# Optimization experiments

Measured on AMD Instinct MI355X. Metric: run time of the kernel, lower is better.

## Reference

```python
import jax, jax.numpy as jnp
from jax import lax
import numpy as np

N_FEATURE = 128
EDGE = 12          # int(sqrt(128) + 1)
BATCH = 131072


def maxpool2(x):
    # 2x2 max pool, stride 2, NCHW
    return lax.reduce_window(x, -jnp.inf, lax.max,
                             (1, 1, 2, 2), (1, 1, 2, 2), 'VALID')


def conv3x3(x, w, b):
    # 3x3 conv, padding=1, NCHW / OIHW
    y = lax.conv_general_dilated(x, w, window_strides=(1, 1),
                                 padding=((1, 1), (1, 1)),
                                 dimension_numbers=('NCHW', 'OIHW', 'NCHW'))
    return y + b[None, :, None, None]


def setup_inputs() -> dict:
    key = jax.random.key(0)
    ks = jax.random.split(key, 9)
    x = jax.random.normal(ks[0], (BATCH, N_FEATURE), dtype=jnp.float32)
    conv1_w = jax.random.normal(ks[1], (3, 1, 3, 3), dtype=jnp.float32) * 0.1
    conv1_b = jnp.zeros((3,), dtype=jnp.float32)
    conv2_w = jax.random.normal(ks[2], (6, 3, 3, 3), dtype=jnp.float32) * 0.1
    conv2_b = jnp.zeros((6,), dtype=jnp.float32)
    fc1_w = jax.random.normal(ks[3], (128, 54), dtype=jnp.float32) * 0.1
    fc1_b = jnp.zeros((128,), dtype=jnp.float32)
    out_w = jax.random.normal(ks[4], (N_FEATURE, 128), dtype=jnp.float32) * 0.1
    out_b = jnp.zeros((N_FEATURE,), dtype=jnp.float32)
    return {"x": x, "conv1_w": conv1_w, "conv1_b": conv1_b,
            "conv2_w": conv2_w, "conv2_b": conv2_b,
            "fc1_w": fc1_w, "fc1_b": fc1_b,
            "out_w": out_w, "out_b": out_b}


def reference(x, conv1_w, conv1_b, conv2_w, conv2_b, fc1_w, fc1_b, out_w, out_b):
    num = x.shape[0]
    n = x.shape[1]                       # 128
    pad = EDGE * EDGE - n                # 16 trailing zeros
    # vectorized transto3D: row-major fill of edge x edge grid, zero-padded tail
    g = jnp.pad(x, ((0, 0), (0, pad))).reshape(num, 1, EDGE, EDGE)
    h = jax.nn.relu(maxpool2(conv3x3(g, conv1_w, conv1_b)))      # [num,3,6,6]
    h = jax.nn.relu(maxpool2(conv3x3(h, conv2_w, conv2_b)))      # [num,6,3,3]
    h = h.reshape(num, 54)
    h = jax.nn.relu(h @ fc1_w.T + fc1_b)                         # [num,128]
    return h @ out_w.T + out_b                                   # [num,128]
```

## Files before the change

### kernel.cpp

```cpp
#include <hip/hip_runtime.h>

typedef unsigned int uint;
typedef unsigned short ushort;

using bf16x8 = __attribute__((ext_vector_type(8))) short;
using f32x4  = __attribute__((ext_vector_type(4))) float;

__device__ __forceinline__ float b2f(ushort u) {
  union { uint i; float f; } v; v.i = ((uint)u) << 16; return v.f;
}
__device__ __forceinline__ ushort f2b(float f) {
  union { float f; uint i; } v; v.f = f;
  uint r = (v.i + 0x7fffu + ((v.i >> 16) & 1u)) >> 16;
  return (ushort)r;
}
__device__ __forceinline__ bf16x8 ldfrag(const ushort* p) {
  union { uint4 u; bf16x8 v; } x; x.u = *(const uint4*)p; return x.v;
}
__device__ __forceinline__ bf16x8 pack8(const float4 a, const float4 b) {
  union { uint4 u; bf16x8 v; } x;
  x.u.x = (uint)f2b(a.x) | ((uint)f2b(a.y) << 16);
  x.u.y = (uint)f2b(a.z) | ((uint)f2b(a.w) << 16);
  x.u.z = (uint)f2b(b.x) | ((uint)f2b(b.y) << 16);
  x.u.w = (uint)f2b(b.z) | ((uint)f2b(b.w) << 16);
  return x.v;
}

template <int Q>
__device__ __forceinline__ void conv_sample(
    const float* __restrict__ xs,
    const float* __restrict__ w1g, const float* __restrict__ b1g,
    const float* __restrict__ w2g, const float* __restrict__ b2g,
    ushort* __restrict__ strow) {
  constexpr int HRLO = (Q == 0) ? 0 : (Q == 1) ? 1 : 3;
  constexpr int HRHI = (Q == 0) ? 2 : (Q == 1) ? 4 : 5;
  constexpr int NR = HRHI - HRLO + 1;
  constexpr int F4LO = (Q == 0) ? 0 : (Q == 1) ? 3 : 15;
  constexpr int F4HI = (Q == 0) ? 20 : 31;

  float xv[128];
#pragma unroll
  for (int i = F4LO; i <= F4HI; ++i) {
    const float4 v = ((const float4*)xs)[i];
    xv[4 * i + 0] = v.x; xv[4 * i + 1] = v.y;
    xv[4 * i + 2] = v.z; xv[4 * i + 3] = v.w;
  }

  float w1[3][9], b1[3];
#pragma unroll
  for (int c = 0; c < 3; ++c) {
    b1[c] = b1g[c];
#pragma unroll
    for (int q = 0; q < 9; ++q) w1[c][q] = w1g[c * 9 + q];
  }

  float h1[3][NR][6];
#pragma unroll
  for (int ri = 0; ri < NR; ++ri) {
    const int hr = HRLO + ri;
#pragma unroll
    for (int pc = 0; pc < 6; ++pc)
#pragma unroll
      for (int ch = 0; ch < 3; ++ch) {
        float m = -3.0e38f;
#pragma unroll
        for (int dr = 0; dr < 2; ++dr)
#pragma unroll
          for (int dc = 0; dc < 2; ++dc) {
            float a = 0.f;
#pragma unroll
            for (int ky = 0; ky < 3; ++ky)
#pragma unroll
              for (int kx = 0; kx < 3; ++kx) {
                const int r = 2 * hr + dr + ky - 1;
                const int c = 2 * pc + dc + kx - 1;
                if (r >= 0 && r < 12 && c >= 0 && c < 12 && (12 * r + c) < 128)
                  a = fmaf(w1[ch][ky * 3 + kx], xv[12 * r + c], a);
              }
            m = fmaxf(m, a);
          }
        h1[ch][ri][pc] = fmaxf(m + b1[ch], 0.f);
      }
  }

#pragma unroll
  for (int o = 0; o < 6; ++o) {
    float w2[27];
#pragma unroll
    for (int q = 0; q < 27; ++q) w2[q] = w2g[o * 27 + q];
    const float bo = b2g[o];
#pragma unroll
    for (int qc = 0; qc < 3; ++qc) {
      float m = -3.0e38f;
#pragma unroll
      for (int dr = 0; dr < 2; ++dr)
#pragma unroll
        for (int dc = 0; dc < 2; ++dc) {
          float a = 0.f;
#pragma unroll
          for (int i = 0; i < 3; ++i)
#pragma unroll
            for (int ky = 0; ky < 3; ++ky)
#pragma unroll
              for (int kx = 0; kx < 3; ++kx) {
                const int yy = 2 * Q + dr + ky - 1;
                const int xx = 2 * qc + dc + kx - 1;
                if (yy >= HRLO && yy <= HRHI && xx >= 0 && xx < 6)
                  a = fmaf(w2[i * 9 + ky * 3 + kx], h1[i][yy - HRLO][xx], a);
              }
          m = fmaxf(m, a);
        }
      strow[o * 9 + Q * 3 + qc] = f2b(fmaxf(m + bo, 0.f));
    }
  }
  if (Q == 2) {
    uint* p = (uint*)(strow + 54);
#pragma unroll
    for (int q = 0; q < 5; ++q) p[q] = 0u;
  }
}

__global__ __launch_bounds__(384, 4) void conv_kernel_r8(
    const float* __restrict__ x,
    const float* __restrict__ w1g, const float* __restrict__ b1g,
    const float* __restrict__ w2g, const float* __restrict__ b2g,
    ushort* __restrict__ h2ws) {
  __shared__ ushort h2st[128][66];

  const int t = threadIdx.x;
  const int s0 = blockIdx.x * 128;
  const int wv = t >> 6;
  const int q  = (wv < 3) ? wv : wv - 3;
  const int sg = (wv < 3) ? 0 : 1;
  const int si = sg * 64 + (t & 63);

  const float* xs = x + (size_t)(s0 + si) * 128;
  ushort* strow = &h2st[si][0];

  if (q == 0)      conv_sample<0>(xs, w1g, b1g, w2g, b2g, strow);
  else if (q == 1) conv_sample<1>(xs, w1g, b1g, w2g, b2g, strow);
  else             conv_sample<2>(xs, w1g, b1g, w2g, b2g, strow);

  __syncthreads();

#pragma unroll
  for (int i = 0; i < 11; ++i) {
    const int f = t + 384 * i;
    if (f < 4096) {
      const int sr = f >> 5, dw = f & 31;
      const uint v = *(const uint*)&h2st[sr][dw * 2];
      ((uint*)h2ws)[((size_t)(s0 + sr) << 5) + dw] = v;
    }
  }
}

__global__ __launch_bounds__(256, 3) void fc_kernel_r8(
    const ushort* __restrict__ h2ws,
    const float* __restrict__ fc1w, const float* __restrict__ fc1b,
    const float* __restrict__ outw, const float* __restrict__ outb,
    float* __restrict__ out) {
  __shared__ __align__(16) ushort w1s[128][72];
  __shared__ __align__(16) ushort tA[128][132];
  __shared__ __align__(16) float fb1[128];
  __shared__ __align__(16) float ob[128];

  const int t = threadIdx.x;
  const int s0 = blockIdx.x * 128;
  const int lane = t & 63, wv = t >> 6;
  const int quad = lane >> 4, lm = lane & 15;

  bf16x8 bh[2][8];
#pragma unroll
  for (int st = 0; st < 8; ++st) {
    const ushort* rp = h2ws + (size_t)(s0 + 16 * st + lm) * 64 + quad * 8;
    bh[0][st] = ldfrag(rp);
    bh[1][st] = ldfrag(rp + 32);
  }

  if (t < 128) { fb1[t] = fc1b[t]; ob[t] = outb[t]; }

#pragma unroll
  for (int i = 0; i < 27; ++i) {
    const int f = t + 256 * i;
    const int n = f / 54, k = f - 54 * n;
    w1s[n][k] = f2b(fc1w[f]);
  }
  if (t < 128) {
    uint* p = (uint*)&w1s[t][54];
#pragma unroll
    for (int q = 0; q < 5; ++q) p[q] = 0u;
  }
  __syncthreads();

  f32x4 acc[2][8];
#pragma unroll
  for (int mt = 0; mt < 2; ++mt)
#pragma unroll
    for (int st = 0; st < 8; ++st) acc[mt][st] = (f32x4){0.f, 0.f, 0.f, 0.f};

#pragma unroll
  for (int kk = 0; kk < 2; ++kk) {
    const int ko = kk * 32 + quad * 8;
    bf16x8 aw[2];
#pragma unroll
    for (int mt = 0; mt < 2; ++mt)
      aw[mt] = ldfrag(&w1s[32 * wv + 16 * mt + lm][ko]);
#pragma unroll
    for (int mt = 0; mt < 2; ++mt)
#pragma unroll
      for (int st = 0; st < 8; ++st)
        acc[mt][st] = __builtin_amdgcn_mfma_f32_16x16x32_bf16(
            aw[mt], bh[kk][st], acc[mt][st], 0, 0, 0);
  }

#pragma unroll
  for (int mt = 0; mt < 2; ++mt) {
    const int jb = 32 * wv + 16 * mt + quad * 4;
    const float4 bj = *(const float4*)&fb1[jb];
#pragma unroll
    for (int st = 0; st < 8; ++st) {
      const int sR = 16 * st + lm;
      const float v0 = fmaxf(acc[mt][st][0] + bj.x, 0.f);
      const float v1 = fmaxf(acc[mt][st][1] + bj.y, 0.f);
      const float v2 = fmaxf(acc[mt][st][2] + bj.z, 0.f);
      const float v3 = fmaxf(acc[mt][st][3] + bj.w, 0.f);
      uint2 pv;
      pv.x = (uint)f2b(v0) | ((uint)f2b(v1) << 16);
      pv.y = (uint)f2b(v2) | ((uint)f2b(v3) << 16);
      *(uint2*)&tA[sR][jb] = pv;
    }
  }
  __syncthreads();

  f32x4 acc2[2][8];
#pragma unroll
  for (int mt = 0; mt < 2; ++mt)
#pragma unroll
    for (int st = 0; st < 8; ++st) acc2[mt][st] = (f32x4){0.f, 0.f, 0.f, 0.f};

#pragma unroll
  for (int kk = 0; kk < 4; ++kk) {
    const int ko = kk * 32 + quad * 8;
    bf16x8 ao[2], bt[8];
#pragma unroll
    for (int mt = 0; mt < 2; ++mt) {
      const float* rp = outw + (size_t)(32 * wv + 16 * mt + lm) * 128 + ko;
      const float4 v0 = *(const float4*)rp;
      const float4 v1 = *(const float4*)(rp + 4);
      ao[mt] = pack8(v0, v1);
    }
#pragma unroll
    for (int st = 0; st < 8; ++st)
      bt[st] = ldfrag(&tA[16 * st + lm][ko]);
#pragma unroll
    for (int mt = 0; mt < 2; ++mt)
#pragma unroll
      for (int st = 0; st < 8; ++st)
        acc2[mt][st] = __builtin_amdgcn_mfma_f32_16x16x32_bf16(
            ao[mt], bt[st], acc2[mt][st], 0, 0, 0);
  }

#pragma unroll
  for (int mt = 0; mt < 2; ++mt) {
    const int obase = 32 * wv + 16 * mt + quad * 4;
    const float4 b4 = *(const float4*)&ob[obase];
#pragma unroll
    for (int st = 0; st < 8; ++st) {
      const int srow = s0 + 16 * st + lm;
      float4 o4;
      o4.x = acc2[mt][st][0] + b4.x;
      o4.y = acc2[mt][st][1] + b4.y;
      o4.z = acc2[mt][st][2] + b4.z;
      o4.w = acc2[mt][st][3] + b4.w;
      *(float4*)&out[(size_t)srow * 128 + obase] = o4;
    }
  }
}

extern "C" void kernel_launch(void* const* d_in, const int* in_sizes, int n_in,
                              void* d_out, int out_size, void* d_ws, size_t ws_size,
                              hipStream_t stream) {
  const float* x    = (const float*)d_in[0];
  const float* w1   = (const float*)d_in[1];
  const float* b1   = (const float*)d_in[2];
  const float* w2   = (const float*)d_in[3];
  const float* b2   = (const float*)d_in[4];
  const float* fc1w = (const float*)d_in[5];
  const float* fc1b = (const float*)d_in[6];
  const float* outw = (const float*)d_in[7];
  const float* outb = (const float*)d_in[8];
  float* outp = (float*)d_out;
  ushort* ws  = (ushort*)d_ws;

  const int N = in_sizes[0] / 128;

  conv_kernel_r8<<<N / 128, 384, 0, stream>>>(x, w1, b1, w2, b2, ws);
  fc_kernel_r8<<<N / 128, 256, 0, stream>>>(ws, fc1w, fc1b, outw, outb, outp);
}
```

Measured before the change: 205.6 us.

## Split conv work by channel across thread groups with LDS-staged conv1 output

Conv work is now split by output channel instead of by output row band. Each of three 128-thread groups computes one conv1 channel for all samples and streams input rows through a rolling 4-row register window. The results go to LDS, and after a barrier each group computes two conv2 output channels. This removes the redundant conv1 recomputation and the large per-thread 128-float input array of the old row-split scheme. In exchange it needs a large LDS buffer (about 56KB plus staging) and an extra barrier, and lowers the occupancy hint from 4 to 3 blocks.

```diff
diff --git a/kernel.cpp b/kernel.cpp
--- a/kernel.cpp
+++ b/kernel.cpp
@@ -26,121 +26,178 @@
   return x.v;
 }
 
-template <int Q>
-__device__ __forceinline__ void conv_sample(
-    const float* __restrict__ xs,
-    const float* __restrict__ w1g, const float* __restrict__ b1g,
-    const float* __restrict__ w2g, const float* __restrict__ b2g,
-    ushort* __restrict__ strow) {
-  constexpr int HRLO = (Q == 0) ? 0 : (Q == 1) ? 1 : 3;
-  constexpr int HRHI = (Q == 0) ? 2 : (Q == 1) ? 4 : 5;
-  constexpr int NR = HRHI - HRLO + 1;
-  constexpr int F4LO = (Q == 0) ? 0 : (Q == 1) ? 3 : 15;
-  constexpr int F4HI = (Q == 0) ? 20 : 31;
-
-  float xv[128];
-#pragma unroll
-  for (int i = F4LO; i <= F4HI; ++i) {
-    const float4 v = ((const float4*)xs)[i];
-    xv[4 * i + 0] = v.x; xv[4 * i + 1] = v.y;
-    xv[4 * i + 2] = v.z; xv[4 * i + 3] = v.w;
-  }
-
-  float w1[3][9], b1[3];
-#pragma unroll
-  for (int c = 0; c < 3; ++c) {
-    b1[c] = b1g[c];
-#pragma unroll
-    for (int q = 0; q < 9; ++q) w1[c][q] = w1g[c * 9 + q];
-  }
-
-  float h1[3][NR][6];
-#pragma unroll
-  for (int ri = 0; ri < NR; ++ri) {
-    const int hr = HRLO + ri;
-#pragma unroll
-    for (int pc = 0; pc < 6; ++pc)
-#pragma unroll
-      for (int ch = 0; ch < 3; ++ch) {
-        float m = -3.0e38f;
-#pragma unroll
-        for (int dr = 0; dr < 2; ++dr)
-#pragma unroll
-          for (int dc = 0; dc < 2; ++dc) {
-            float a = 0.f;
-#pragma unroll
-            for (int ky = 0; ky < 3; ++ky)
-#pragma unroll
-              for (int kx = 0; kx < 3; ++kx) {
-                const int r = 2 * hr + dr + ky - 1;
-                const int c = 2 * pc + dc + kx - 1;
-                if (r >= 0 && r < 12 && c >= 0 && c < 12 && (12 * r + c) < 128)
-                  a = fmaf(w1[ch][ky * 3 + kx], xv[12 * r + c], a);
-              }
-            m = fmaxf(m, a);
+template <int R>
+__device__ __forceinline__ void load_row(const float* __restrict__ xs,
+                                         float (&d)[12]) {
+  if constexpr (R >= 11) {
+#pragma unroll
+    for (int c = 0; c < 12; ++c) d[c] = 0.f;
+  } else if constexpr (R == 10) {
+    const float4 a = *(const float4*)(xs + 120);
+    const float4 b = *(const float4*)(xs + 124);
+    d[0] = a.x; d[1] = a.y; d[2] = a.z; d[3] = a.w;
+    d[4] = b.x; d[5] = b.y; d[6] = b.z; d[7] = b.w;
+    d[8] = 0.f; d[9] = 0.f; d[10] = 0.f; d[11] = 0.f;
+  } else {
+#pragma unroll
+    for (int q = 0; q < 3; ++q) {
+      const float4 v = *(const float4*)(xs + 12 * R + 4 * q);
+      d[4 * q + 0] = v.x; d[4 * q + 1] = v.y;
+      d[4 * q + 2] = v.z; d[4 * q + 3] = v.w;
+    }
+  }
+}
+
+template <int PR>
+__device__ __forceinline__ void conv1_band(const float* __restrict__ xs,
+                                           float (&xr)[4][12],
+                                           const float (&w1r)[9], float b1v,
+                                           float* __restrict__ hlrow) {
+  if constexpr (PR >= 1) {
+    load_row<2 * PR + 1>(xs, xr[(2 * PR + 1) & 3]);
+    if constexpr (2 * PR + 2 <= 11)
+      load_row<2 * PR + 2>(xs, xr[(2 * PR + 2) & 3]);
+  }
+  float out[6];
+#pragma unroll
+  for (int pc = 0; pc < 6; ++pc) {
+    float m = -3.0e38f;
+#pragma unroll
+    for (int dr = 0; dr < 2; ++dr)
+#pragma unroll
+      for (int dc = 0; dc < 2; ++dc) {
+        float a = 0.f;
+#pragma unroll
+        for (int ky = 0; ky < 3; ++ky)
+#pragma unroll
+          for (int kx = 0; kx < 3; ++kx) {
+            const int y = 2 * PR + dr + ky - 1;
+            const int cc = 2 * pc + dc + kx - 1;
+            if (y >= 0 && y < 12 && cc >= 0 && cc < 12 &&
+                (12 * y + cc) < 128)
+              a = fmaf(w1r[ky * 3 + kx], xr[y & 3][cc], a);
           }
-        h1[ch][ri][pc] = fmaxf(m + b1[ch], 0.f);
+        m = fmaxf(m, a);
       }
-  }
-
-#pragma unroll
-  for (int o = 0; o < 6; ++o) {
-    float w2[27];
-#pragma unroll
-    for (int q = 0; q < 27; ++q) w2[q] = w2g[o * 27 + q];
-    const float bo = b2g[o];
-#pragma unroll
-    for (int qc = 0; qc < 3; ++qc) {
-      float m = -3.0e38f;
-#pragma unroll
-      for (int dr = 0; dr < 2; ++dr)
-#pragma unroll
-        for (int dc = 0; dc < 2; ++dc) {
-          float a = 0.f;
-#pragma unroll
-          for (int i = 0; i < 3; ++i)
-#pragma unroll
-            for (int ky = 0; ky < 3; ++ky)
-#pragma unroll
-              for (int kx = 0; kx < 3; ++kx) {
-                const int yy = 2 * Q + dr + ky - 1;
-                const int xx = 2 * qc + dc + kx - 1;
-                if (yy >= HRLO && yy <= HRHI && xx >= 0 && xx < 6)
-                  a = fmaf(w2[i * 9 + ky * 3 + kx], h1[i][yy - HRLO][xx], a);
-              }
-          m = fmaxf(m, a);
-        }
-      strow[o * 9 + Q * 3 + qc] = f2b(fmaxf(m + bo, 0.f));
-    }
-  }
-  if (Q == 2) {
-    uint* p = (uint*)(strow + 54);
-#pragma unroll
-    for (int q = 0; q < 5; ++q) p[q] = 0u;
-  }
-}
-
-__global__ __launch_bounds__(384, 4) void conv_kernel_r8(
+    out[pc] = fmaxf(m + b1v, 0.f);
+  }
+#pragma unroll
+  for (int q = 0; q < 3; ++q)
+    *(float2*)&hlrow[PR * 6 + 2 * q] = make_float2(out[2 * q], out[2 * q + 1]);
+}
+
+__global__ __launch_bounds__(384, 3) void conv_kernel_r9(
     const float* __restrict__ x,
     const float* __restrict__ w1g, const float* __restrict__ b1g,
     const float* __restrict__ w2g, const float* __restrict__ b2g,
     ushort* __restrict__ h2ws) {
+  __shared__ float hl[128 * 110];
   __shared__ ushort h2st[128][66];
 
   const int t = threadIdx.x;
   const int s0 = blockIdx.x * 128;
-  const int wv = t >> 6;
-  const int q  = (wv < 3) ? wv : wv - 3;
-  const int sg = (wv < 3) ? 0 : 1;
-  const int si = sg * 64 + (t & 63);
+  const int si = t & 127;
+  const int grp = __builtin_amdgcn_readfirstlane(t >> 7);
 
   const float* xs = x + (size_t)(s0 + si) * 128;
-  ushort* strow = &h2st[si][0];
-
-  if (q == 0)      conv_sample<0>(xs, w1g, b1g, w2g, b2g, strow);
-  else if (q == 1) conv_sample<1>(xs, w1g, b1g, w2g, b2g, strow);
-  else             conv_sample<2>(xs, w1g, b1g, w2g, b2g, strow);
-
+
+  {
+    float w1r[9];
+#pragma unroll
+    for (int q = 0; q < 9; ++q) w1r[q] = w1g[grp * 9 + q];
+    const float b1v = b1g[grp];
+
+    float xr[4][12];
+    load_row<0>(xs, xr[0]);
+    load_row<1>(xs, xr[1]);
+    load_row<2>(xs, xr[2]);
+    float* hlrow = &hl[si * 110 + grp * 36];
+
+    conv1_band<0>(xs, xr, w1r, b1v, hlrow);
+    conv1_band<1>(xs, xr, w1r, b1v, hlrow);
+    conv1_band<2>(xs, xr, w1r, b1v, hlrow);
+    conv1_band<3>(xs, xr, w1r, b1v, hlrow);
+    conv1_band<4>(xs, xr, w1r, b1v, hlrow);
+    conv1_band<5>(xs, xr, w1r, b1v, hlrow);
+  }
+  __syncthreads();
+
+  {
+    const int o0 = 2 * grp;
+    float w2a[27], w2b[27];
+#pragma unroll
+    for (int q = 0; q < 27; ++q) {
+      w2a[q] = w2g[o0 * 27 + q];
+      w2b[q] = w2g[(o0 + 1) * 27 + q];
+    }
+    const float b2a = b2g[o0], b2b = b2g[o0 + 1];
+    const float* hbase = &hl[si * 110];
+
+#pragma unroll
+    for (int qr = 0; qr < 3; ++qr) {
+      const int lo = (qr == 0) ? 0 : 2 * qr - 1;
+      const int hi = (qr == 2) ? 5 : 2 * qr + 2;
+      float s[2][3][4];
+#pragma unroll
+      for (int oo = 0; oo < 2; ++oo)
+#pragma unroll
+        for (int qc = 0; qc < 3; ++qc)
+#pragma unroll
+          for (int p = 0; p < 4; ++p) s[oo][qc][p] = 0.f;
+
+#pragma unroll
+      for (int i = 0; i < 3; ++i) {
+        float hwv[4][6];
+#pragma unroll
+        for (int rr = 0; rr < 4; ++rr) {
+          if (lo + rr <= hi) {
+#pragma unroll
+            for (int q = 0; q < 3; ++q) {
+              const float2 p2 =
+                  *(const float2*)&hbase[i * 36 + (lo + rr) * 6 + 2 * q];
+              hwv[rr][2 * q] = p2.x; hwv[rr][2 * q + 1] = p2.y;
+            }
+          }
+        }
+#pragma unroll
+        for (int ky = 0; ky < 3; ++ky)
+#pragma unroll
+          for (int kx = 0; kx < 3; ++kx) {
+            const float wa = w2a[i * 9 + ky * 3 + kx];
+            const float wb = w2b[i * 9 + ky * 3 + kx];
+#pragma unroll
+            for (int dr = 0; dr < 2; ++dr) {
+              const int y = 2 * qr + dr + ky - 1;
+              if (y < lo || y > hi) continue;
+#pragma unroll
+              for (int qc = 0; qc < 3; ++qc)
+#pragma unroll
+                for (int dc = 0; dc < 2; ++dc) {
+                  const int xx = 2 * qc + dc + kx - 1;
+                  if (xx < 0 || xx > 5) continue;
+                  const float h = hwv[y - lo][xx];
+                  s[0][qc][dr * 2 + dc] = fmaf(wa, h, s[0][qc][dr * 2 + dc]);
+                  s[1][qc][dr * 2 + dc] = fmaf(wb, h, s[1][qc][dr * 2 + dc]);
+                }
+            }
+          }
+      }
+#pragma unroll
+      for (int oo = 0; oo < 2; ++oo)
+#pragma unroll
+        for (int qc = 0; qc < 3; ++qc) {
+          const float m = fmaxf(fmaxf(s[oo][qc][0], s[oo][qc][1]),
+                                fmaxf(s[oo][qc][2], s[oo][qc][3]));
+          const float bv = oo ? b2b : b2a;
+          h2st[si][(o0 + oo) * 9 + qr * 3 + qc] = f2b(fmaxf(m + bv, 0.f));
+        }
+    }
+    if (grp == 2) {
+      uint* p = (uint*)&h2st[si][54];
+#pragma unroll
+      for (int q = 0; q < 5; ++q) p[q] = 0u;
+    }
+  }
   __syncthreads();
 
 #pragma unroll
@@ -154,7 +211,7 @@
   }
 }
 
-__global__ __launch_bounds__(256, 3) void fc_kernel_r8(
+__global__ __launch_bounds__(256, 3) void fc_kernel_r9(
     const ushort* __restrict__ h2ws,
     const float* __restrict__ fc1w, const float* __restrict__ fc1b,
     const float* __restrict__ outw, const float* __restrict__ outb,
@@ -294,6 +351,6 @@
 
   const int N = in_sizes[0] / 128;
 
-  conv_kernel_r8<<<N / 128, 384, 0, stream>>>(x, w1, b1, w2, b2, ws);
-  fc_kernel_r8<<<N / 128, 256, 0, stream>>>(ws, fc1w, fc1b, outw, outb, outp);
-}
+  conv_kernel_r9<<<N / 128, 384, 0, stream>>>(x, w1, b1, w2, b2, ws);
+  fc_kernel_r9<<<N / 128, 256, 0, stream>>>(ws, fc1w, fc1b, outw, outb, outp);
+}
```

Measured after the change: 196.8 us. 1.04x faster.
